# Kernel tuning notes

Hardware: AMD Instinct MI355X
Metric: run time of the kernel (lower is better)

Reference implementation:

```python
import jax, jax.numpy as jnp
import numpy as np

N_NODES = 50000
N_EDGES = 800000
FEAT = 128
HIDDEN = 128
N_GRAPHS = 128


def setup_inputs() -> dict:
    key = jax.random.key(0)
    ks = jax.random.split(key, 12)
    x = jax.random.normal(ks[0], (N_NODES, FEAT), dtype=jnp.float32)
    # edges with no self loops (original add_remaining_self_loops drops existing
    # self loops and re-adds all of them; generating loop-free edges keeps the
    # reference simple and exactly equivalent)
    row = jax.random.randint(ks[1], (N_EDGES,), 0, N_NODES)
    off = jax.random.randint(ks[2], (N_EDGES,), 1, N_NODES)
    col = (row + off) % N_NODES
    edge_index = jnp.stack([row, col]).astype(jnp.int64)
    batch = jnp.sort(jax.random.randint(ks[3], (N_NODES,), 0, N_GRAPHS)).astype(jnp.int64)
    def glorot(k, fan_in, fan_out):
        s = np.sqrt(6.0 / (fan_in + fan_out))
        return jax.random.uniform(k, (fan_in, fan_out), jnp.float32, -s, s)
    W0 = glorot(ks[4], FEAT, HIDDEN)
    W1 = glorot(ks[5], HIDDEN, HIDDEN)
    W2 = glorot(ks[6], HIDDEN, HIDDEN)
    b0 = jnp.zeros((HIDDEN,), jnp.float32)
    b1 = jnp.zeros((HIDDEN,), jnp.float32)
    b2 = jnp.zeros((HIDDEN,), jnp.float32)
    return {"x": x, "edge_index": edge_index, "batch": batch,
            "W0": W0, "b0": b0, "W1": W1, "b1": b1, "W2": W2, "b2": b2}


def _gcn_norm(edge_index, num_nodes):
    # add self loops, compute symmetric normalization coeffs per edge
    loops = jnp.arange(num_nodes, dtype=edge_index.dtype)
    row = jnp.concatenate([edge_index[0], loops])
    col = jnp.concatenate([edge_index[1], loops])
    w = jnp.ones(row.shape[0], jnp.float32)
    deg = jax.ops.segment_sum(w, col, num_segments=num_nodes)
    dis = jnp.where(deg > 0, jax.lax.rsqrt(jnp.maximum(deg, 1e-30)), 0.0)
    norm = dis[row] * dis[col]
    return row, col, norm


def _gcn_layer(x, row, col, norm, W, b, num_nodes):
    h = x @ W                               # [N, H]
    msg = norm[:, None] * h[row]            # gather + scale  [E+N, H]
    out = jax.ops.segment_sum(msg, col, num_segments=num_nodes) + b
    return jax.nn.relu(out)


def reference(x, edge_index, batch, W0, b0, W1, b1, W2, b2):
    n = x.shape[0]
    row, col, norm = _gcn_norm(edge_index, n)
    x1 = _gcn_layer(x, row, col, norm, W0, b0, n)
    x2 = _gcn_layer(x1, row, col, norm, W1, b1, n)
    x3 = _gcn_layer(x2, row, col, norm, W2, b2, n)
    pools = [jax.ops.segment_sum(xi, batch, num_segments=N_GRAPHS)
             for xi in (x1, x2, x3)]
    global_rep = jnp.concatenate(pools, axis=1)  # [G, 3*H]
    return (global_rep, x3)
```

## Files before the change

### kernel.cpp

```cpp
#include <hip/hip_runtime.h>
#include <hip/hip_fp16.h>

#define N_NODES 50000
#define N_EDGES 800000
#define F 128
#define NG 128
#define POOL_W (3*F)
#define SCAN_CHUNK 1024
#define SCAN_BLKS ((N_NODES + SCAN_CHUNK - 1) / SCAN_CHUNK)

typedef __attribute__((ext_vector_type(8))) short short8;
typedef __attribute__((ext_vector_type(4))) float f32x4;

__device__ __forceinline__ unsigned short f2bf(float f) {
    unsigned u = __float_as_uint(f);
    u = (u + 0x7FFFu + ((u >> 16) & 1u)) >> 16;
    return (unsigned short)u;
}
__device__ __forceinline__ float bflo(unsigned u) { return __uint_as_float(u << 16); }
__device__ __forceinline__ float bfhi(unsigned u) { return __uint_as_float(u & 0xFFFF0000u); }
__device__ __forceinline__ float nrm_of(unsigned u) {
    return __half2float(__ushort_as_half((unsigned short)(u & 0xFFFFu)));
}

__global__ void k_init(int* __restrict__ cnt, float* __restrict__ pool,
                       const float* __restrict__ W0, const float* __restrict__ W1,
                       const float* __restrict__ W2, unsigned short* __restrict__ WT) {
    int i = blockIdx.x * 256 + threadIdx.x;
    if (i < N_NODES) cnt[i] = 0;
    if (i < NG * POOL_W) {
        pool[i] = 0.0f;
        int w = i >> 14, r = i & 16383;
        int k = r >> 7, c = r & 127;
        const float* W = (w == 0) ? W0 : (w == 1) ? W1 : W2;
        WT[(size_t)w * F * F + c * F + k] = f2bf(W[r]);
    }
}

__global__ void k_hist(const int* __restrict__ col, int* __restrict__ cnt,
                       unsigned short* __restrict__ seq) {
    int e = blockIdx.x * 256 + threadIdx.x;
    if (e < N_EDGES) seq[e] = (unsigned short)atomicAdd(&cnt[col[e]], 1);
}

__global__ __launch_bounds__(256) void k_scan_red(const int* __restrict__ cnt,
                                                  int* __restrict__ part) {
    __shared__ int wsum[4];
    int i4 = blockIdx.x * SCAN_CHUNK + threadIdx.x * 4;
    int s;
    if (i4 + 3 < N_NODES) {
        int4 v = *(const int4*)&cnt[i4];
        s = v.x + v.y + v.z + v.w;
    } else {
        s = 0;
        #pragma unroll
        for (int j = 0; j < 4; ++j) if (i4 + j < N_NODES) s += cnt[i4 + j];
    }
    #pragma unroll
    for (int o = 32; o > 0; o >>= 1) s += __shfl_xor(s, o, 64);
    int lane = threadIdx.x & 63, w = threadIdx.x >> 6;
    if (lane == 0) wsum[w] = s;
    __syncthreads();
    if (threadIdx.x == 0) part[blockIdx.x] = wsum[0] + wsum[1] + wsum[2] + wsum[3];
}

__global__ void k_scan_off(const int* __restrict__ part, int* __restrict__ off) {
    int i = threadIdx.x;
    int v = (i < SCAN_BLKS) ? part[i] : 0;
    int s = v;
    #pragma unroll
    for (int o = 1; o < 64; o <<= 1) {
        int t = __shfl_up(s, o, 64);
        if (i >= o) s += t;
    }
    if (i < SCAN_BLKS) off[i] = s - v;
}

__global__ __launch_bounds__(256) void k_scan_fin(const int* __restrict__ cnt,
                                                  const int* __restrict__ off,
                                                  int* __restrict__ rowptr,
                                                  float* __restrict__ dis) {
    __shared__ int wsum[4];
    int i4 = blockIdx.x * SCAN_CHUNK + threadIdx.x * 4;
    int v[4];
    #pragma unroll
    for (int j = 0; j < 4; ++j) v[j] = (i4 + j < N_NODES) ? cnt[i4 + j] : 0;
    int ts = v[0] + v[1] + v[2] + v[3];
    int lane = threadIdx.x & 63, w = threadIdx.x >> 6;
    int incl = ts;
    #pragma unroll
    for (int o = 1; o < 64; o <<= 1) {
        int t = __shfl_up(incl, o, 64);
        if (lane >= o) incl += t;
    }
    if (lane == 63) wsum[w] = incl;
    __syncthreads();
    if (threadIdx.x == 0) {
        int a = 0;
        #pragma unroll
        for (int t = 0; t < 4; ++t) { int b = wsum[t]; wsum[t] = a; a += b; }
    }
    __syncthreads();
    int base = off[blockIdx.x] + wsum[w] + (incl - ts);
    int pre = 0;
    #pragma unroll
    for (int j = 0; j < 4; ++j) {
        int i = i4 + j;
        if (i <= N_NODES) rowptr[i] = base + pre;
        if (i < N_NODES) dis[i] = rsqrtf((float)v[j] + 1.0f);
        pre += v[j];
    }
}

__global__ void k_fill(const int* __restrict__ row, const int* __restrict__ col,
                       const unsigned short* __restrict__ seq,
                       const int* __restrict__ rowptr, const float* __restrict__ dis,
                       unsigned* __restrict__ csr) {
    int e = blockIdx.x * 256 + threadIdx.x;
    if (e >= N_EDGES) return;
    int r = row[e], c = col[e];
    int p = rowptr[c] + (int)seq[e];
    unsigned short hn = __half_as_ushort(__float2half_rn(dis[r] * dis[c]));
    csr[p] = ((unsigned)r << 16) | (unsigned)hn;
}

template <typename AIN>
__global__ __launch_bounds__(256) void k_gemm(const AIN* __restrict__ A,
                                              const unsigned short* __restrict__ WT,
                                              unsigned short* __restrict__ H) {
    __shared__ unsigned short sWT[F * 136];
    for (int t = threadIdx.x; t < F * 16; t += 256) {
        int c = t >> 4, ch = t & 15;
        *(uint4*)&sWT[c * 136 + ch * 8] = *(const uint4*)&WT[(size_t)c * F + ch * 8];
    }
    __syncthreads();

    int wave = threadIdx.x >> 6, lane = threadIdx.x & 63;
    int m = lane & 15, q = lane >> 4;
    int row = blockIdx.x * 64 + wave * 16 + m;
    int arow = (row < N_NODES) ? row : (N_NODES - 1);

    f32x4 acc[8];
    #pragma unroll
    for (int c = 0; c < 8; ++c) acc[c] = 0.f;

    #pragma unroll
    for (int kk = 0; kk < 4; ++kk) {
        int k0 = kk * 32 + q * 8;
        short8 a;
        if constexpr (sizeof(AIN) == 4) {
            const float* ap = &A[(size_t)arow * F + k0];
            float4 a0 = *(const float4*)ap;
            float4 a1 = *(const float4*)(ap + 4);
            a[0] = (short)f2bf(a0.x); a[1] = (short)f2bf(a0.y);
            a[2] = (short)f2bf(a0.z); a[3] = (short)f2bf(a0.w);
            a[4] = (short)f2bf(a1.x); a[5] = (short)f2bf(a1.y);
            a[6] = (short)f2bf(a1.z); a[7] = (short)f2bf(a1.w);
        } else {
            a = *(const short8*)&A[(size_t)arow * F + k0];
        }
        #pragma unroll
        for (int c = 0; c < 8; ++c) {
            short8 b = *(const short8*)&sWT[(c * 16 + m) * 136 + k0];
            acc[c] = __builtin_amdgcn_mfma_f32_16x16x32_bf16(a, b, acc[c], 0, 0, 0);
        }
    }

    int rbase = blockIdx.x * 64 + wave * 16 + q * 4;
    #pragma unroll
    for (int c = 0; c < 8; ++c) {
        #pragma unroll
        for (int r = 0; r < 4; ++r) {
            int rr = rbase + r;
            if (rr < N_NODES) H[(size_t)rr * F + c * 16 + m] = f2bf(acc[c][r]);
        }
    }
}

template <typename OUT>
__global__ __launch_bounds__(256) void k_agg(const unsigned short* __restrict__ h,
                                             const float* __restrict__ dis,
                                             const int* __restrict__ rowptr,
                                             const unsigned* __restrict__ csr,
                                             const float* __restrict__ bias,
                                             const int* __restrict__ batch,
                                             OUT* __restrict__ xout,
                                             float* __restrict__ pool) {
    int wave = threadIdx.x >> 6;
    int lane = threadIdx.x & 63;
    int g = lane >> 4;
    int l = lane & 15;
    int node = blockIdx.x * 4 + wave;

    float acc[8] = {0.f, 0.f, 0.f, 0.f, 0.f, 0.f, 0.f, 0.f};

    int s = rowptr[node], e = rowptr[node + 1];
    int i = s + g;
    unsigned c0 = (i      < e) ? csr[i]      : 0u;
    unsigned c1 = (i + 4  < e) ? csr[i + 4]  : 0u;
    unsigned c2 = (i + 8  < e) ? csr[i + 8]  : 0u;
    unsigned c3 = (i + 12 < e) ? csr[i + 12] : 0u;
    while (i < e) {
        uint4 v0 = *(const uint4*)&h[(size_t)(c0 >> 16) * F + l * 8];
        uint4 v1 = *(const uint4*)&h[(size_t)(c1 >> 16) * F + l * 8];
        uint4 v2 = *(const uint4*)&h[(size_t)(c2 >> 16) * F + l * 8];
        uint4 v3 = *(const uint4*)&h[(size_t)(c3 >> 16) * F + l * 8];
        float n0 = nrm_of(c0), n1 = nrm_of(c1), n2 = nrm_of(c2), n3 = nrm_of(c3);
        c0 = (i + 16 < e) ? csr[i + 16] : 0u;
        c1 = (i + 20 < e) ? csr[i + 20] : 0u;
        c2 = (i + 24 < e) ? csr[i + 24] : 0u;
        c3 = (i + 28 < e) ? csr[i + 28] : 0u;
        acc[0] = fmaf(n0, bflo(v0.x), acc[0]);
        acc[1] = fmaf(n0, bfhi(v0.x), acc[1]);
        acc[2] = fmaf(n0, bflo(v0.y), acc[2]);
        acc[3] = fmaf(n0, bfhi(v0.y), acc[3]);
        acc[4] = fmaf(n0, bflo(v0.z), acc[4]);
        acc[5] = fmaf(n0, bfhi(v0.z), acc[5]);
        acc[6] = fmaf(n0, bflo(v0.w), acc[6]);
        acc[7] = fmaf(n0, bfhi(v0.w), acc[7]);
        acc[0] = fmaf(n1, bflo(v1.x), acc[0]);
        acc[1] = fmaf(n1, bfhi(v1.x), acc[1]);
        acc[2] = fmaf(n1, bflo(v1.y), acc[2]);
        acc[3] = fmaf(n1, bfhi(v1.y), acc[3]);
        acc[4] = fmaf(n1, bflo(v1.z), acc[4]);
        acc[5] = fmaf(n1, bfhi(v1.z), acc[5]);
        acc[6] = fmaf(n1, bflo(v1.w), acc[6]);
        acc[7] = fmaf(n1, bfhi(v1.w), acc[7]);
        acc[0] = fmaf(n2, bflo(v2.x), acc[0]);
        acc[1] = fmaf(n2, bfhi(v2.x), acc[1]);
        acc[2] = fmaf(n2, bflo(v2.y), acc[2]);
        acc[3] = fmaf(n2, bfhi(v2.y), acc[3]);
        acc[4] = fmaf(n2, bflo(v2.z), acc[4]);
        acc[5] = fmaf(n2, bfhi(v2.z), acc[5]);
        acc[6] = fmaf(n2, bflo(v2.w), acc[6]);
        acc[7] = fmaf(n2, bfhi(v2.w), acc[7]);
        acc[0] = fmaf(n3, bflo(v3.x), acc[0]);
        acc[1] = fmaf(n3, bfhi(v3.x), acc[1]);
        acc[2] = fmaf(n3, bflo(v3.y), acc[2]);
        acc[3] = fmaf(n3, bfhi(v3.y), acc[3]);
        acc[4] = fmaf(n3, bflo(v3.z), acc[4]);
        acc[5] = fmaf(n3, bfhi(v3.z), acc[5]);
        acc[6] = fmaf(n3, bflo(v3.w), acc[6]);
        acc[7] = fmaf(n3, bfhi(v3.w), acc[7]);
        i += 16;
    }

    #pragma unroll
    for (int j = 0; j < 8; ++j) {
        acc[j] += __shfl_xor(acc[j], 16, 64);
        acc[j] += __shfl_xor(acc[j], 32, 64);
    }

    float dd = dis[node]; dd = dd * dd;
    uint4 sv = *(const uint4*)&h[(size_t)node * F + l * 8];
    acc[0] = fmaf(dd, bflo(sv.x), acc[0]);
    acc[1] = fmaf(dd, bfhi(sv.x), acc[1]);
    acc[2] = fmaf(dd, bflo(sv.y), acc[2]);
    acc[3] = fmaf(dd, bfhi(sv.y), acc[3]);
    acc[4] = fmaf(dd, bflo(sv.z), acc[4]);
    acc[5] = fmaf(dd, bfhi(sv.z), acc[5]);
    acc[6] = fmaf(dd, bflo(sv.w), acc[6]);
    acc[7] = fmaf(dd, bfhi(sv.w), acc[7]);
    float4 ba = *(const float4*)&bias[l * 8];
    float4 bb = *(const float4*)&bias[l * 8 + 4];
    acc[0] = fmaxf(acc[0] + ba.x, 0.f);
    acc[1] = fmaxf(acc[1] + ba.y, 0.f);
    acc[2] = fmaxf(acc[2] + ba.z, 0.f);
    acc[3] = fmaxf(acc[3] + ba.w, 0.f);
    acc[4] = fmaxf(acc[4] + bb.x, 0.f);
    acc[5] = fmaxf(acc[5] + bb.y, 0.f);
    acc[6] = fmaxf(acc[6] + bb.z, 0.f);
    acc[7] = fmaxf(acc[7] + bb.w, 0.f);

    if (g == 0) {
        if constexpr (sizeof(OUT) == 2) {
            uint4 o;
            o.x = (unsigned)f2bf(acc[0]) | ((unsigned)f2bf(acc[1]) << 16);
            o.y = (unsigned)f2bf(acc[2]) | ((unsigned)f2bf(acc[3]) << 16);
            o.z = (unsigned)f2bf(acc[4]) | ((unsigned)f2bf(acc[5]) << 16);
            o.w = (unsigned)f2bf(acc[6]) | ((unsigned)f2bf(acc[7]) << 16);
            *(uint4*)&xout[(size_t)node * F + l * 8] = o;
        } else {
            *(float4*)&xout[(size_t)node * F + l * 8] =
                make_float4(acc[0], acc[1], acc[2], acc[3]);
            *(float4*)&xout[(size_t)node * F + l * 8 + 4] =
                make_float4(acc[4], acc[5], acc[6], acc[7]);
        }
    }

    __shared__ float red[4][F];
    __shared__ int gsh[4];
    if (lane == 0) gsh[wave] = batch[node];
    if (g == 0) {
        *(float4*)&red[wave][l * 8]     = make_float4(acc[0], acc[1], acc[2], acc[3]);
        *(float4*)&red[wave][l * 8 + 4] = make_float4(acc[4], acc[5], acc[6], acc[7]);
    }
    __syncthreads();
    int g0 = gsh[0];
    bool uni = (gsh[1] == g0) & (gsh[2] == g0) & (gsh[3] == g0);
    if (uni) {
        if (threadIdx.x < F) {
            float ssum = red[0][threadIdx.x] + red[1][threadIdx.x]
                       + red[2][threadIdx.x] + red[3][threadIdx.x];
            atomicAdd(&pool[(size_t)g0 * POOL_W + threadIdx.x], ssum);
        }
    } else if (g == 0) {
        int gg = gsh[wave];
        #pragma unroll
        for (int j = 0; j < 8; ++j)
            atomicAdd(&pool[(size_t)gg * POOL_W + l * 8 + j], acc[j]);
    }
}

extern "C" void kernel_launch(void* const* d_in, const int* in_sizes, int n_in,
                              void* d_out, int out_size, void* d_ws, size_t ws_size,
                              hipStream_t stream) {
    const float* x    = (const float*)d_in[0];
    const int*   erow = (const int*)d_in[1];
    const int*   ecol = erow + N_EDGES;
    const int*   batch= (const int*)d_in[2];
    const float* W0   = (const float*)d_in[3];
    const float* b0   = (const float*)d_in[4];
    const float* W1   = (const float*)d_in[5];
    const float* b1   = (const float*)d_in[6];
    const float* W2   = (const float*)d_in[7];
    const float* b2   = (const float*)d_in[8];

    float* pool = (float*)d_out;
    float* x3   = (float*)d_out + NG * POOL_W;

    char* p = (char*)d_ws;
    auto carve = [&](size_t bytes) { char* q = p; p += (bytes + 255) & ~(size_t)255; return q; };
    float*          dis    = (float*)carve(N_NODES * 4);
    int*            cnt    = (int*)  carve(N_NODES * 4);
    int*            rowptr = (int*)  carve((N_NODES + 1) * 4);
    unsigned short* seq    = (unsigned short*)carve((size_t)N_EDGES * 2);
    int*            part   = (int*)  carve(SCAN_BLKS * 4);
    int*            offs   = (int*)  carve(SCAN_BLKS * 4);
    unsigned*       csr    = (unsigned*)carve((size_t)N_EDGES * 4);
    unsigned short* WT     = (unsigned short*)carve((size_t)3 * F * F * 2);
    unsigned short* h      = (unsigned short*)carve((size_t)N_NODES * F * 2);
    unsigned short* B      = (unsigned short*)carve((size_t)N_NODES * F * 2);

    const int nodeBlk = (N_NODES + 255) / 256;
    const int edgeBlk = (N_EDGES + 255) / 256;
    const int aggBlk  = N_NODES / 4;
    const int gemmBlk = (N_NODES + 63) / 64;

    k_init<<<nodeBlk, 256, 0, stream>>>(cnt, pool, W0, W1, W2, WT);
    k_hist<<<edgeBlk, 256, 0, stream>>>(ecol, cnt, seq);
    k_scan_red<<<SCAN_BLKS, 256, 0, stream>>>(cnt, part);
    k_scan_off<<<1, 64, 0, stream>>>(part, offs);
    k_scan_fin<<<SCAN_BLKS, 256, 0, stream>>>(cnt, offs, rowptr, dis);
    k_fill<<<edgeBlk, 256, 0, stream>>>(erow, ecol, seq, rowptr, dis, csr);

    k_gemm<float><<<gemmBlk, 256, 0, stream>>>(x, WT + 0 * F * F, h);
    k_agg<unsigned short><<<aggBlk, 256, 0, stream>>>(h, dis, rowptr, csr, b0, batch, B, pool + 0 * F);

    k_gemm<unsigned short><<<gemmBlk, 256, 0, stream>>>(B, WT + 1 * F * F, h);
    k_agg<unsigned short><<<aggBlk, 256, 0, stream>>>(h, dis, rowptr, csr, b1, batch, B, pool + 1 * F);

    k_gemm<unsigned short><<<gemmBlk, 256, 0, stream>>>(B, WT + 2 * F * F, h);
    k_agg<float><<<aggBlk, 256, 0, stream>>>(h, dis, rowptr, csr, b2, batch, x3, pool + 2 * F);
}
```

Measured before the change: 219.0 us.

## Switch intermediates and aggregation to packed fp16, fuse scan offset, process two edges per thread

Replaces bf16 storage and fp32 accumulation with fp16 everywhere: fp16 MFMA in the GEMM, and packed half2 multiply-add accumulation in the aggregation kernel, including the cross-lane reduction, self-loop term, bias and ReLU. It also folds the single-block scan-offset kernel into the scan finalise kernel and makes the histogram and CSR fill kernels handle two edges per thread with vector loads. The aim is fewer ALU ops in the gather loop and one fewer launch. The cost is fp16 accumulation over neighbour sums, which risks precision loss or overflow compared with fp32 accumulation.

```diff
diff --git a/kernel.cpp b/kernel.cpp
--- a/kernel.cpp
+++ b/kernel.cpp
@@ -9,23 +9,23 @@
 #define SCAN_CHUNK 1024
 #define SCAN_BLKS ((N_NODES + SCAN_CHUNK - 1) / SCAN_CHUNK)
 
-typedef __attribute__((ext_vector_type(8))) short short8;
+typedef _Float16 f16x2 __attribute__((ext_vector_type(2)));
+typedef _Float16 f16x8 __attribute__((ext_vector_type(8)));
 typedef __attribute__((ext_vector_type(4))) float f32x4;
 
-__device__ __forceinline__ unsigned short f2bf(float f) {
-    unsigned u = __float_as_uint(f);
-    u = (u + 0x7FFFu + ((u >> 16) & 1u)) >> 16;
-    return (unsigned short)u;
-}
-__device__ __forceinline__ float bflo(unsigned u) { return __uint_as_float(u << 16); }
-__device__ __forceinline__ float bfhi(unsigned u) { return __uint_as_float(u & 0xFFFF0000u); }
-__device__ __forceinline__ float nrm_of(unsigned u) {
-    return __half2float(__ushort_as_half((unsigned short)(u & 0xFFFFu)));
+union U32H2 { unsigned u; f16x2 h; };
+
+__device__ __forceinline__ f16x2 h2(unsigned u) { U32H2 t; t.u = u; return t.h; }
+__device__ __forceinline__ unsigned u_of(f16x2 h) { U32H2 t; t.h = h; return t.u; }
+__device__ __forceinline__ unsigned short f2h16(float f) {
+    return __half_as_ushort(__float2half_rn(f));
 }
 
 __global__ void k_init(int* __restrict__ cnt, float* __restrict__ pool,
                        const float* __restrict__ W0, const float* __restrict__ W1,
-                       const float* __restrict__ W2, unsigned short* __restrict__ WT) {
+                       const float* __restrict__ W2, unsigned short* __restrict__ WT,
+                       const float* __restrict__ b0, const float* __restrict__ b1,
+                       const float* __restrict__ b2, unsigned short* __restrict__ bH) {
     int i = blockIdx.x * 256 + threadIdx.x;
     if (i < N_NODES) cnt[i] = 0;
     if (i < NG * POOL_W) {
@@ -33,14 +33,22 @@
         int w = i >> 14, r = i & 16383;
         int k = r >> 7, c = r & 127;
         const float* W = (w == 0) ? W0 : (w == 1) ? W1 : W2;
-        WT[(size_t)w * F * F + c * F + k] = f2bf(W[r]);
+        WT[(size_t)w * F * F + c * F + k] = f2h16(W[r]);
+    }
+    if (i < 3 * F) {
+        const float* b = (i < F) ? b0 : (i < 2 * F) ? b1 : b2;
+        bH[i] = f2h16(b[i & 127]);
     }
 }
 
 __global__ void k_hist(const int* __restrict__ col, int* __restrict__ cnt,
                        unsigned short* __restrict__ seq) {
-    int e = blockIdx.x * 256 + threadIdx.x;
-    if (e < N_EDGES) seq[e] = (unsigned short)atomicAdd(&cnt[col[e]], 1);
+    int e2 = (blockIdx.x * 256 + threadIdx.x) * 2;
+    if (e2 >= N_EDGES) return;
+    int2 cc = *(const int2*)&col[e2];
+    unsigned short s0 = (unsigned short)atomicAdd(&cnt[cc.x], 1);
+    unsigned short s1 = (unsigned short)atomicAdd(&cnt[cc.y], 1);
+    *(ushort2*)&seq[e2] = make_ushort2(s0, s1);
 }
 
 __global__ __launch_bounds__(256) void k_scan_red(const int* __restrict__ cnt,
@@ -64,29 +72,30 @@
     if (threadIdx.x == 0) part[blockIdx.x] = wsum[0] + wsum[1] + wsum[2] + wsum[3];
 }
 
-__global__ void k_scan_off(const int* __restrict__ part, int* __restrict__ off) {
-    int i = threadIdx.x;
-    int v = (i < SCAN_BLKS) ? part[i] : 0;
-    int s = v;
-    #pragma unroll
-    for (int o = 1; o < 64; o <<= 1) {
-        int t = __shfl_up(s, o, 64);
-        if (i >= o) s += t;
-    }
-    if (i < SCAN_BLKS) off[i] = s - v;
-}
-
 __global__ __launch_bounds__(256) void k_scan_fin(const int* __restrict__ cnt,
-                                                  const int* __restrict__ off,
+                                                  const int* __restrict__ part,
                                                   int* __restrict__ rowptr,
                                                   float* __restrict__ dis) {
     __shared__ int wsum[4];
+    __shared__ int sBase;
+    int lane = threadIdx.x & 63, w = threadIdx.x >> 6;
+
+    if (w == 0) {
+        int v = (lane < SCAN_BLKS) ? part[lane] : 0;
+        int s = v;
+        #pragma unroll
+        for (int o = 1; o < 64; o <<= 1) {
+            int t = __shfl_up(s, o, 64);
+            if (lane >= o) s += t;
+        }
+        if (lane == (int)blockIdx.x) sBase = s - v;
+    }
+
     int i4 = blockIdx.x * SCAN_CHUNK + threadIdx.x * 4;
     int v[4];
     #pragma unroll
     for (int j = 0; j < 4; ++j) v[j] = (i4 + j < N_NODES) ? cnt[i4 + j] : 0;
     int ts = v[0] + v[1] + v[2] + v[3];
-    int lane = threadIdx.x & 63, w = threadIdx.x >> 6;
     int incl = ts;
     #pragma unroll
     for (int o = 1; o < 64; o <<= 1) {
@@ -101,7 +110,7 @@
         for (int t = 0; t < 4; ++t) { int b = wsum[t]; wsum[t] = a; a += b; }
     }
     __syncthreads();
-    int base = off[blockIdx.x] + wsum[w] + (incl - ts);
+    int base = sBase + wsum[w] + (incl - ts);
     int pre = 0;
     #pragma unroll
     for (int j = 0; j < 4; ++j) {
@@ -116,12 +125,15 @@
                        const unsigned short* __restrict__ seq,
                        const int* __restrict__ rowptr, const float* __restrict__ dis,
                        unsigned* __restrict__ csr) {
-    int e = blockIdx.x * 256 + threadIdx.x;
-    if (e >= N_EDGES) return;
-    int r = row[e], c = col[e];
-    int p = rowptr[c] + (int)seq[e];
-    unsigned short hn = __half_as_ushort(__float2half_rn(dis[r] * dis[c]));
-    csr[p] = ((unsigned)r << 16) | (unsigned)hn;
+    int e2 = (blockIdx.x * 256 + threadIdx.x) * 2;
+    if (e2 >= N_EDGES) return;
+    int2 rr = *(const int2*)&row[e2];
+    int2 cc = *(const int2*)&col[e2];
+    ushort2 ss = *(const ushort2*)&seq[e2];
+    int p0 = rowptr[cc.x] + (int)ss.x;
+    csr[p0] = ((unsigned)rr.x << 16) | (unsigned)f2h16(dis[rr.x] * dis[cc.x]);
+    int p1 = rowptr[cc.y] + (int)ss.y;
+    csr[p1] = ((unsigned)rr.y << 16) | (unsigned)f2h16(dis[rr.y] * dis[cc.y]);
 }
 
 template <typename AIN>
@@ -147,22 +159,22 @@
     #pragma unroll
     for (int kk = 0; kk < 4; ++kk) {
         int k0 = kk * 32 + q * 8;
-        short8 a;
+        f16x8 a;
         if constexpr (sizeof(AIN) == 4) {
             const float* ap = &A[(size_t)arow * F + k0];
             float4 a0 = *(const float4*)ap;
             float4 a1 = *(const float4*)(ap + 4);
-            a[0] = (short)f2bf(a0.x); a[1] = (short)f2bf(a0.y);
-            a[2] = (short)f2bf(a0.z); a[3] = (short)f2bf(a0.w);
-            a[4] = (short)f2bf(a1.x); a[5] = (short)f2bf(a1.y);
-            a[6] = (short)f2bf(a1.z); a[7] = (short)f2bf(a1.w);
+            a[0] = (_Float16)a0.x; a[1] = (_Float16)a0.y;
+            a[2] = (_Float16)a0.z; a[3] = (_Float16)a0.w;
+            a[4] = (_Float16)a1.x; a[5] = (_Float16)a1.y;
+            a[6] = (_Float16)a1.z; a[7] = (_Float16)a1.w;
         } else {
-            a = *(const short8*)&A[(size_t)arow * F + k0];
+            a = *(const f16x8*)&A[(size_t)arow * F + k0];
         }
         #pragma unroll
         for (int c = 0; c < 8; ++c) {
-            short8 b = *(const short8*)&sWT[(c * 16 + m) * 136 + k0];
-            acc[c] = __builtin_amdgcn_mfma_f32_16x16x32_bf16(a, b, acc[c], 0, 0, 0);
+            f16x8 b = *(const f16x8*)&sWT[(c * 16 + m) * 136 + k0];
+            acc[c] = __builtin_amdgcn_mfma_f32_16x16x32_f16(a, b, acc[c], 0, 0, 0);
         }
     }
 
@@ -172,7 +184,7 @@
         #pragma unroll
         for (int r = 0; r < 4; ++r) {
             int rr = rbase + r;
-            if (rr < N_NODES) H[(size_t)rr * F + c * 16 + m] = f2bf(acc[c][r]);
+            if (rr < N_NODES) H[(size_t)rr * F + c * 16 + m] = f2h16(acc[c][r]);
         }
     }
 }
@@ -182,7 +194,7 @@
                                              const float* __restrict__ dis,
                                              const int* __restrict__ rowptr,
                                              const unsigned* __restrict__ csr,
-                                             const float* __restrict__ bias,
+                                             const unsigned short* __restrict__ bH,
                                              const int* __restrict__ batch,
                                              OUT* __restrict__ xout,
                                              float* __restrict__ pool) {
@@ -192,7 +204,7 @@
     int l = lane & 15;
     int node = blockIdx.x * 4 + wave;
 
-    float acc[8] = {0.f, 0.f, 0.f, 0.f, 0.f, 0.f, 0.f, 0.f};
+    f16x2 a0 = {0, 0}, a1 = {0, 0}, a2 = {0, 0}, a3 = {0, 0};
 
     int s = rowptr[node], e = rowptr[node + 1];
     int i = s + g;
@@ -205,86 +217,61 @@
         uint4 v1 = *(const uint4*)&h[(size_t)(c1 >> 16) * F + l * 8];
         uint4 v2 = *(const uint4*)&h[(size_t)(c2 >> 16) * F + l * 8];
         uint4 v3 = *(const uint4*)&h[(size_t)(c3 >> 16) * F + l * 8];
-        float n0 = nrm_of(c0), n1 = nrm_of(c1), n2 = nrm_of(c2), n3 = nrm_of(c3);
+        f16x2 n0 = h2(__builtin_amdgcn_perm(c0, c0, 0x01000100));
+        f16x2 n1 = h2(__builtin_amdgcn_perm(c1, c1, 0x01000100));
+        f16x2 n2 = h2(__builtin_amdgcn_perm(c2, c2, 0x01000100));
+        f16x2 n3 = h2(__builtin_amdgcn_perm(c3, c3, 0x01000100));
         c0 = (i + 16 < e) ? csr[i + 16] : 0u;
         c1 = (i + 20 < e) ? csr[i + 20] : 0u;
         c2 = (i + 24 < e) ? csr[i + 24] : 0u;
         c3 = (i + 28 < e) ? csr[i + 28] : 0u;
-        acc[0] = fmaf(n0, bflo(v0.x), acc[0]);
-        acc[1] = fmaf(n0, bfhi(v0.x), acc[1]);
-        acc[2] = fmaf(n0, bflo(v0.y), acc[2]);
-        acc[3] = fmaf(n0, bfhi(v0.y), acc[3]);
-        acc[4] = fmaf(n0, bflo(v0.z), acc[4]);
-        acc[5] = fmaf(n0, bfhi(v0.z), acc[5]);
-        acc[6] = fmaf(n0, bflo(v0.w), acc[6]);
-        acc[7] = fmaf(n0, bfhi(v0.w), acc[7]);
-        acc[0] = fmaf(n1, bflo(v1.x), acc[0]);
-        acc[1] = fmaf(n1, bfhi(v1.x), acc[1]);
-        acc[2] = fmaf(n1, bflo(v1.y), acc[2]);
-        acc[3] = fmaf(n1, bfhi(v1.y), acc[3]);
-        acc[4] = fmaf(n1, bflo(v1.z), acc[4]);
-        acc[5] = fmaf(n1, bfhi(v1.z), acc[5]);
-        acc[6] = fmaf(n1, bflo(v1.w), acc[6]);
-        acc[7] = fmaf(n1, bfhi(v1.w), acc[7]);
-        acc[0] = fmaf(n2, bflo(v2.x), acc[0]);
-        acc[1] = fmaf(n2, bfhi(v2.x), acc[1]);
-        acc[2] = fmaf(n2, bflo(v2.y), acc[2]);
-        acc[3] = fmaf(n2, bfhi(v2.y), acc[3]);
-        acc[4] = fmaf(n2, bflo(v2.z), acc[4]);
-        acc[5] = fmaf(n2, bfhi(v2.z), acc[5]);
-        acc[6] = fmaf(n2, bflo(v2.w), acc[6]);
-        acc[7] = fmaf(n2, bfhi(v2.w), acc[7]);
-        acc[0] = fmaf(n3, bflo(v3.x), acc[0]);
-        acc[1] = fmaf(n3, bfhi(v3.x), acc[1]);
-        acc[2] = fmaf(n3, bflo(v3.y), acc[2]);
-        acc[3] = fmaf(n3, bfhi(v3.y), acc[3]);
-        acc[4] = fmaf(n3, bflo(v3.z), acc[4]);
-        acc[5] = fmaf(n3, bfhi(v3.z), acc[5]);
-        acc[6] = fmaf(n3, bflo(v3.w), acc[6]);
-        acc[7] = fmaf(n3, bfhi(v3.w), acc[7]);
+        a0 += n0 * h2(v0.x); a1 += n0 * h2(v0.y); a2 += n0 * h2(v0.z); a3 += n0 * h2(v0.w);
+        a0 += n1 * h2(v1.x); a1 += n1 * h2(v1.y); a2 += n1 * h2(v1.z); a3 += n1 * h2(v1.w);
+        a0 += n2 * h2(v2.x); a1 += n2 * h2(v2.y); a2 += n2 * h2(v2.z); a3 += n2 * h2(v2.w);
+        a0 += n3 * h2(v3.x); a1 += n3 * h2(v3.y); a2 += n3 * h2(v3.z); a3 += n3 * h2(v3.w);
         i += 16;
     }
 
-    #pragma unroll
-    for (int j = 0; j < 8; ++j) {
-        acc[j] += __shfl_xor(acc[j], 16, 64);
-        acc[j] += __shfl_xor(acc[j], 32, 64);
-    }
-
-    float dd = dis[node]; dd = dd * dd;
+    f16x2 acc[4] = {a0, a1, a2, a3};
+    #pragma unroll
+    for (int j = 0; j < 4; ++j) {
+        U32H2 t; t.h = acc[j];
+        U32H2 r1; r1.u = (unsigned)__shfl_xor((int)t.u, 16, 64);
+        t.h = t.h + r1.h;
+        U32H2 r2; r2.u = (unsigned)__shfl_xor((int)t.u, 32, 64);
+        t.h = t.h + r2.h;
+        acc[j] = t.h;
+    }
+
+    float df = dis[node];
+    _Float16 ddh = (_Float16)(df * df);
+    f16x2 dd2 = {ddh, ddh};
     uint4 sv = *(const uint4*)&h[(size_t)node * F + l * 8];
-    acc[0] = fmaf(dd, bflo(sv.x), acc[0]);
-    acc[1] = fmaf(dd, bfhi(sv.x), acc[1]);
-    acc[2] = fmaf(dd, bflo(sv.y), acc[2]);
-    acc[3] = fmaf(dd, bfhi(sv.y), acc[3]);
-    acc[4] = fmaf(dd, bflo(sv.z), acc[4]);
-    acc[5] = fmaf(dd, bfhi(sv.z), acc[5]);
-    acc[6] = fmaf(dd, bflo(sv.w), acc[6]);
-    acc[7] = fmaf(dd, bfhi(sv.w), acc[7]);
-    float4 ba = *(const float4*)&bias[l * 8];
-    float4 bb = *(const float4*)&bias[l * 8 + 4];
-    acc[0] = fmaxf(acc[0] + ba.x, 0.f);
-    acc[1] = fmaxf(acc[1] + ba.y, 0.f);
-    acc[2] = fmaxf(acc[2] + ba.z, 0.f);
-    acc[3] = fmaxf(acc[3] + ba.w, 0.f);
-    acc[4] = fmaxf(acc[4] + bb.x, 0.f);
-    acc[5] = fmaxf(acc[5] + bb.y, 0.f);
-    acc[6] = fmaxf(acc[6] + bb.z, 0.f);
-    acc[7] = fmaxf(acc[7] + bb.w, 0.f);
+    acc[0] += dd2 * h2(sv.x); acc[1] += dd2 * h2(sv.y);
+    acc[2] += dd2 * h2(sv.z); acc[3] += dd2 * h2(sv.w);
+    uint4 bu = *(const uint4*)&bH[l * 8];
+    f16x2 z = {(_Float16)0.f, (_Float16)0.f};
+    acc[0] = __builtin_elementwise_max(acc[0] + h2(bu.x), z);
+    acc[1] = __builtin_elementwise_max(acc[1] + h2(bu.y), z);
+    acc[2] = __builtin_elementwise_max(acc[2] + h2(bu.z), z);
+    acc[3] = __builtin_elementwise_max(acc[3] + h2(bu.w), z);
+
+    float pf[8];
+    #pragma unroll
+    for (int j = 0; j < 4; ++j) {
+        pf[2 * j]     = (float)acc[j][0];
+        pf[2 * j + 1] = (float)acc[j][1];
+    }
 
     if (g == 0) {
         if constexpr (sizeof(OUT) == 2) {
-            uint4 o;
-            o.x = (unsigned)f2bf(acc[0]) | ((unsigned)f2bf(acc[1]) << 16);
-            o.y = (unsigned)f2bf(acc[2]) | ((unsigned)f2bf(acc[3]) << 16);
-            o.z = (unsigned)f2bf(acc[4]) | ((unsigned)f2bf(acc[5]) << 16);
-            o.w = (unsigned)f2bf(acc[6]) | ((unsigned)f2bf(acc[7]) << 16);
+            uint4 o = make_uint4(u_of(acc[0]), u_of(acc[1]), u_of(acc[2]), u_of(acc[3]));
             *(uint4*)&xout[(size_t)node * F + l * 8] = o;
         } else {
             *(float4*)&xout[(size_t)node * F + l * 8] =
-                make_float4(acc[0], acc[1], acc[2], acc[3]);
+                make_float4(pf[0], pf[1], pf[2], pf[3]);
             *(float4*)&xout[(size_t)node * F + l * 8 + 4] =
-                make_float4(acc[4], acc[5], acc[6], acc[7]);
+                make_float4(pf[4], pf[5], pf[6], pf[7]);
         }
     }
 
@@ -292,8 +279,8 @@
     __shared__ int gsh[4];
     if (lane == 0) gsh[wave] = batch[node];
     if (g == 0) {
-        *(float4*)&red[wave][l * 8]     = make_float4(acc[0], acc[1], acc[2], acc[3]);
-        *(float4*)&red[wave][l * 8 + 4] = make_float4(acc[4], acc[5], acc[6], acc[7]);
+        *(float4*)&red[wave][l * 8]     = make_float4(pf[0], pf[1], pf[2], pf[3]);
+        *(float4*)&red[wave][l * 8 + 4] = make_float4(pf[4], pf[5], pf[6], pf[7]);
     }
     __syncthreads();
     int g0 = gsh[0];
@@ -308,7 +295,7 @@
         int gg = gsh[wave];
         #pragma unroll
         for (int j = 0; j < 8; ++j)
-            atomicAdd(&pool[(size_t)gg * POOL_W + l * 8 + j], acc[j]);
+            atomicAdd(&pool[(size_t)gg * POOL_W + l * 8 + j], pf[j]);
     }
 }
 
@@ -336,30 +323,29 @@
     int*            rowptr = (int*)  carve((N_NODES + 1) * 4);
     unsigned short* seq    = (unsigned short*)carve((size_t)N_EDGES * 2);
     int*            part   = (int*)  carve(SCAN_BLKS * 4);
-    int*            offs   = (int*)  carve(SCAN_BLKS * 4);
     unsigned*       csr    = (unsigned*)carve((size_t)N_EDGES * 4);
     unsigned short* WT     = (unsigned short*)carve((size_t)3 * F * F * 2);
+    unsigned short* bH     = (unsigned short*)carve((size_t)3 * F * 2);
     unsigned short* h      = (unsigned short*)carve((size_t)N_NODES * F * 2);
     unsigned short* B      = (unsigned short*)carve((size_t)N_NODES * F * 2);
 
-    const int nodeBlk = (N_NODES + 255) / 256;
-    const int edgeBlk = (N_EDGES + 255) / 256;
-    const int aggBlk  = N_NODES / 4;
-    const int gemmBlk = (N_NODES + 63) / 64;
-
-    k_init<<<nodeBlk, 256, 0, stream>>>(cnt, pool, W0, W1, W2, WT);
-    k_hist<<<edgeBlk, 256, 0, stream>>>(ecol, cnt, seq);
+    const int nodeBlk  = (N_NODES + 255) / 256;
+    const int edge2Blk = (N_EDGES / 2 + 255) / 256;
+    const int aggBlk   = N_NODES / 4;
+    const int gemmBlk  = (N_NODES + 63) / 64;
+
+    k_init<<<nodeBlk, 256, 0, stream>>>(cnt, pool, W0, W1, W2, WT, b0, b1, b2, bH);
+    k_hist<<<edge2Blk, 256, 0, stream>>>(ecol, cnt, seq);
     k_scan_red<<<SCAN_BLKS, 256, 0, stream>>>(cnt, part);
-    k_scan_off<<<1, 64, 0, stream>>>(part, offs);
-    k_scan_fin<<<SCAN_BLKS, 256, 0, stream>>>(cnt, offs, rowptr, dis);
-    k_fill<<<edgeBlk, 256, 0, stream>>>(erow, ecol, seq, rowptr, dis, csr);
+    k_scan_fin<<<SCAN_BLKS, 256, 0, stream>>>(cnt, part, rowptr, dis);
+    k_fill<<<edge2Blk, 256, 0, stream>>>(erow, ecol, seq, rowptr, dis, csr);
 
     k_gemm<float><<<gemmBlk, 256, 0, stream>>>(x, WT + 0 * F * F, h);
-    k_agg<unsigned short><<<aggBlk, 256, 0, stream>>>(h, dis, rowptr, csr, b0, batch, B, pool + 0 * F);
+    k_agg<unsigned short><<<aggBlk, 256, 0, stream>>>(h, dis, rowptr, csr, bH + 0 * F, batch, B, pool + 0 * F);
 
     k_gemm<unsigned short><<<gemmBlk, 256, 0, stream>>>(B, WT + 1 * F * F, h);
-    k_agg<unsigned short><<<aggBlk, 256, 0, stream>>>(h, dis, rowptr, csr, b1, batch, B, pool + 1 * F);
+    k_agg<unsigned short><<<aggBlk, 256, 0, stream>>>(h, dis, rowptr, csr, bH + 1 * F, batch, B, pool + 1 * F);
 
     k_gemm<unsigned short><<<gemmBlk, 256, 0, stream>>>(B, WT + 2 * F * F, h);
-    k_agg<float><<<aggBlk, 256, 0, stream>>>(h, dis, rowptr, csr, b2, batch, x3, pool + 2 * F);
-}
+    k_agg<float><<<aggBlk, 256, 0, stream>>>(h, dis, rowptr, csr, bH + 2 * F, batch, x3, pool + 2 * F);
+}
```

After: 216.2 us. About the same (-1.3%).
